# Kernel tuning notes

Hardware: AMD Instinct MI355X
Metric: run time of the kernel (lower is better)

## Reference

```python
import jax, jax.numpy as jnp
import numpy as np

N, NFEAT, NHID, NHID2 = 10000, 512, 256, 128


def setup_inputs() -> dict:
    key = jax.random.key(0)
    k1, k2, k3, k4 = jax.random.split(key, 4)
    x = jax.random.normal(k1, (N, NFEAT), dtype=jnp.float32)
    # sparse-ish row-normalized adjacency, stored dense (as the module's spmm operand)
    raw = jax.random.uniform(k2, (N, N), dtype=jnp.float32)
    adj = jnp.where(raw > 0.995, raw, 0.0)
    adj = adj / jnp.maximum(adj.sum(axis=1, keepdims=True), 1e-6)
    W1 = jax.random.normal(k3, (NFEAT, NHID), dtype=jnp.float32) / np.sqrt(NFEAT)
    b1 = jnp.zeros((NHID,), dtype=jnp.float32)
    W2 = jax.random.normal(k4, (NHID, NHID2), dtype=jnp.float32) / np.sqrt(NHID)
    b2 = jnp.zeros((NHID2,), dtype=jnp.float32)
    return {"x": x, "adj": adj, "W1": W1, "b1": b1, "W2": W2, "b2": b2}


def gcn_conv(x, adj, W, b):
    # standard Kipf GCNConv: adj @ (x @ W) + b
    return adj @ (x @ W) + b


def reference(x, adj, W1, b1, W2, b2):
    h = jax.nn.relu(gcn_conv(x, adj, W1, b1))
    # dropout is identity in inference mode (training=False)
    h = jax.nn.relu(gcn_conv(h, adj, W2, b2))
    return h
```

## Files before the change

kernel.cpp:

```cpp
#include <hip/hip_runtime.h>

#define N_NODES 10000
#define NFEAT   512
#define NHID    256
#define NHID2   128
#define CAP     128

typedef __attribute__((ext_vector_type(8))) short bf16x8;
typedef __attribute__((ext_vector_type(4))) float f32x4;
typedef __attribute__((ext_vector_type(2))) int   i32x2;

__device__ __forceinline__ ushort f2bf(float f){
  union { float f; unsigned u; } v; v.f = f;
  unsigned r = v.u + 0x7FFFu + ((v.u >> 16) & 1u);
  return (ushort)(r >> 16);
}
__device__ __forceinline__ float bf2f(ushort u){
  union { unsigned u; float f; } v; v.u = ((unsigned)u) << 16; return v.f;
}

__launch_bounds__(256)
__global__ void k_scan_cvt(const float* __restrict__ adj, const float* __restrict__ x,
                           const float* __restrict__ W1, const float* __restrict__ W2,
                           ushort* __restrict__ xb, ushort* __restrict__ w1t,
                           ushort* __restrict__ w2t, int* __restrict__ row_nnz,
                           i32x2* __restrict__ pja){
  const int b = blockIdx.x, t = threadIdx.x;

  if (b >= N_NODES){
    if (b < 15000){
      int i = ((b - N_NODES) * 256 + t) * 4;
      float4 q = *(const float4*)(x + i);
      ushort4 o; o.x = f2bf(q.x); o.y = f2bf(q.y); o.z = f2bf(q.z); o.w = f2bf(q.w);
      *(ushort4*)(xb + i) = o;
    } else if (b < 15512){
      int id = (b - 15000) * 256 + t;
      int n = id >> 9, k = id & 511;
      w1t[id] = f2bf(W1[k * NHID + n]);
    } else {
      int id = (b - 15512) * 256 + t;
      int n = id >> 8, k = id & 255;
      w2t[id] = f2bf(W2[k * NHID2 + n]);
    }
    return;
  }

  const int r = b;
  const int lane = t & 63, w = t >> 6;
  const float* row = adj + (size_t)r * N_NODES;
  __shared__ int swave[4];

  f32x4 vals[10];
  #pragma unroll
  for (int v = 0; v < 9; v++)
    vals[v] = __builtin_nontemporal_load((const f32x4*)(row + v * 1024 + t * 4));
  vals[9] = (f32x4){0.f, 0.f, 0.f, 0.f};
  if (t < 196) vals[9] = __builtin_nontemporal_load((const f32x4*)(row + 9216 + t * 4));

  int cnt = 0;
  #pragma unroll
  for (int v = 0; v < 10; v++)
    cnt += (vals[v].x != 0.f) + (vals[v].y != 0.f) + (vals[v].z != 0.f) + (vals[v].w != 0.f);

  int incl = cnt;
  #pragma unroll
  for (int d = 1; d < 64; d <<= 1){
    int u = __shfl_up(incl, d, 64);
    if (lane >= d) incl += u;
  }
  if (lane == 63) swave[w] = incl;
  __syncthreads();
  int woff = 0, total = 0;
  #pragma unroll
  for (int i = 0; i < 4; i++){
    int s = swave[i];
    total += s;
    if (i < w) woff += s;
  }
  int pos = woff + incl - cnt;

  #pragma unroll
  for (int v = 0; v < 10; v++){
    float q[4] = {vals[v].x, vals[v].y, vals[v].z, vals[v].w};
    #pragma unroll
    for (int e = 0; e < 4; e++){
      if (q[e] != 0.f && pos < CAP){
        pja[(size_t)r * CAP + pos] = (i32x2){(v * 1024 + t * 4 + e) << 8, __float_as_int(q[e])};
        pos++;
      }
    }
  }
  if (t == 0) row_nnz[r] = min(total, CAP);
}

__launch_bounds__(256)
__global__ void k_gemm1(const ushort* __restrict__ A, const ushort* __restrict__ Bt,
                        ushort* __restrict__ xw1_lo, ushort* __restrict__ xw1_hi){
  const int lane = threadIdx.x & 63;
  const int w    = threadIdx.x >> 6;
  const int wr   = w >> 1, wc = w & 1;
  const int r16  = lane & 15;
  const int kg   = lane >> 4;
  const int row0 = blockIdx.x * 64 + wr * 32;
  const int col0 = blockIdx.y * 64 + wc * 32;

  int arow[2], bcol[2];
  #pragma unroll
  for (int r = 0; r < 2; r++){
    int ar = row0 + r * 16 + r16;
    arow[r] = (ar >= N_NODES) ? (N_NODES - 1) : ar;
  }
  #pragma unroll
  for (int c = 0; c < 2; c++) bcol[c] = col0 + c * 16 + r16;

  f32x4 acc[2][2];
  #pragma unroll
  for (int r = 0; r < 2; r++)
    #pragma unroll
    for (int c = 0; c < 2; c++)
      acc[r][c] = (f32x4){0.f, 0.f, 0.f, 0.f};

  bf16x8 aA[2], bA[2], aB[2], bB[2];
  auto LOADF = [&](bf16x8* a, bf16x8* bb, int k0){
    #pragma unroll
    for (int r = 0; r < 2; r++)
      a[r] = *(const bf16x8*)(A + (size_t)arow[r] * NFEAT + k0 + kg * 8);
    #pragma unroll
    for (int c = 0; c < 2; c++)
      bb[c] = *(const bf16x8*)(Bt + (size_t)bcol[c] * NFEAT + k0 + kg * 8);
  };
  auto MM = [&](bf16x8* a, bf16x8* bb){
    #pragma unroll
    for (int r = 0; r < 2; r++)
      #pragma unroll
      for (int c = 0; c < 2; c++)
        acc[r][c] = __builtin_amdgcn_mfma_f32_16x16x32_bf16(a[r], bb[c], acc[r][c], 0, 0, 0);
  };

  LOADF(aA, bA, 0);
  #pragma unroll
  for (int k0 = 0; k0 < NFEAT; k0 += 64){
    if (k0 + 32 < NFEAT) LOADF(aB, bB, k0 + 32);
    MM(aA, bA);
    if (k0 + 64 < NFEAT) LOADF(aA, bA, k0 + 64);
    if (k0 + 32 < NFEAT) MM(aB, bB);
  }

  ushort* dst = (blockIdx.y < 2) ? xw1_lo : xw1_hi;
  const int cbase = (blockIdx.y < 2) ? 0 : 128;
  #pragma unroll
  for (int r = 0; r < 2; r++)
    #pragma unroll
    for (int c = 0; c < 2; c++){
      int col = col0 + c * 16 + r16 - cbase;
      #pragma unroll
      for (int i = 0; i < 4; i++){
        int row = row0 + r * 16 + kg * 4 + i;
        if (row < N_NODES) dst[(size_t)row * 128 + col] = f2bf(acc[r][c][i]);
      }
    }
}

__launch_bounds__(256)
__global__ void k_agg1(const int* __restrict__ row_nnz, const i32x2* __restrict__ pja,
                       const ushort* __restrict__ xw1_lo, const ushort* __restrict__ xw1_hi,
                       const float* __restrict__ b1, ushort* __restrict__ Hb){
  const int half = blockIdx.x & 1;
  const int r0   = (blockIdx.x >> 1) * 16;
  const int t = threadIdx.x;
  __shared__ i32x2 sl[16][CAP];
  __shared__ int   sn[16];
  if (t < 16) sn[t] = row_nnz[r0 + t];
  #pragma unroll
  for (int e = 0; e < 8; e++){
    int idx = t + e * 256;
    int rr = idx >> 7, kk = idx & (CAP - 1);
    sl[rr][kk] = pja[(size_t)(r0 + rr) * CAP + kk];
  }
  __syncthreads();

  const int wv = t >> 6, lane = t & 63;
  const char* table = (const char*)(half ? xw1_hi : xw1_lo);
  const float bias0 = b1[half * 128 + lane * 2 + 0];
  const float bias1 = b1[half * 128 + lane * 2 + 1];

  #pragma unroll
  for (int rr = wv; rr < 16; rr += 4){
    const int n = sn[rr];
    float a0 = 0.f, a1 = 0.f;
    for (int k = 0; k < n; k++){
      i32x2 p = sl[rr][k];
      uint pk = *(const uint*)(table + p.x + lane * 4);
      float a = __int_as_float(p.y);
      a0 += a * bf2f((ushort)(pk & 0xffff));
      a1 += a * bf2f((ushort)(pk >> 16));
    }
    uint o = ((uint)f2bf(fmaxf(a1 + bias1, 0.f)) << 16) | (uint)f2bf(fmaxf(a0 + bias0, 0.f));
    *(uint*)(Hb + (size_t)(r0 + rr) * NHID + half * 128 + lane * 2) = o;
  }
}

__launch_bounds__(256)
__global__ void k_gemm2(const ushort* __restrict__ A, const ushort* __restrict__ Bt,
                        ushort* __restrict__ C){
  const int lane = threadIdx.x & 63;
  const int w    = threadIdx.x >> 6;
  const int wr   = w >> 1, wc = w & 1;
  const int r16  = lane & 15;
  const int kg   = lane >> 4;
  const int row0 = blockIdx.x * 64 + wr * 32;
  const int col0 = blockIdx.y * 64 + wc * 32;

  int arow[2], bcol[2];
  #pragma unroll
  for (int r = 0; r < 2; r++){
    int ar = row0 + r * 16 + r16;
    arow[r] = (ar >= N_NODES) ? (N_NODES - 1) : ar;
  }
  #pragma unroll
  for (int c = 0; c < 2; c++) bcol[c] = col0 + c * 16 + r16;

  f32x4 acc[2][2];
  #pragma unroll
  for (int r = 0; r < 2; r++)
    #pragma unroll
    for (int c = 0; c < 2; c++)
      acc[r][c] = (f32x4){0.f, 0.f, 0.f, 0.f};

  bf16x8 aA[2], bA[2], aB[2], bB[2];
  auto LOADF = [&](bf16x8* a, bf16x8* bb, int k0){
    #pragma unroll
    for (int r = 0; r < 2; r++)
      a[r] = *(const bf16x8*)(A + (size_t)arow[r] * NHID + k0 + kg * 8);
    #pragma unroll
    for (int c = 0; c < 2; c++)
      bb[c] = *(const bf16x8*)(Bt + (size_t)bcol[c] * NHID + k0 + kg * 8);
  };
  auto MM = [&](bf16x8* a, bf16x8* bb){
    #pragma unroll
    for (int r = 0; r < 2; r++)
      #pragma unroll
      for (int c = 0; c < 2; c++)
        acc[r][c] = __builtin_amdgcn_mfma_f32_16x16x32_bf16(a[r], bb[c], acc[r][c], 0, 0, 0);
  };

  LOADF(aA, bA, 0);
  #pragma unroll
  for (int k0 = 0; k0 < NHID; k0 += 64){
    if (k0 + 32 < NHID) LOADF(aB, bB, k0 + 32);
    MM(aA, bA);
    if (k0 + 64 < NHID) LOADF(aA, bA, k0 + 64);
    if (k0 + 32 < NHID) MM(aB, bB);
  }

  #pragma unroll
  for (int r = 0; r < 2; r++)
    #pragma unroll
    for (int c = 0; c < 2; c++){
      int col = col0 + c * 16 + r16;
      #pragma unroll
      for (int i = 0; i < 4; i++){
        int row = row0 + r * 16 + kg * 4 + i;
        if (row < N_NODES) C[(size_t)row * NHID2 + col] = f2bf(acc[r][c][i]);
      }
    }
}

__launch_bounds__(256)
__global__ void k_agg2(const int* __restrict__ row_nnz, const i32x2* __restrict__ pja,
                       const ushort* __restrict__ hw2b, const float* __restrict__ b2,
                       float* __restrict__ out){
  const int r0 = blockIdx.x * 8;
  const int t = threadIdx.x;
  __shared__ i32x2 sl[8][CAP];
  __shared__ int   sn[8];
  if (t < 8) sn[t] = row_nnz[r0 + t];
  #pragma unroll
  for (int e = 0; e < 4; e++){
    int idx = t + e * 256;
    int rr = idx >> 7, kk = idx & (CAP - 1);
    sl[rr][kk] = pja[(size_t)(r0 + rr) * CAP + kk];
  }
  __syncthreads();

  const int wv = t >> 6, lane = t & 63;
  const char* table = (const char*)hw2b;
  const float bias0 = b2[lane * 2 + 0];
  const float bias1 = b2[lane * 2 + 1];

  #pragma unroll
  for (int rr = wv; rr < 8; rr += 4){
    const int n = sn[rr];
    float a0 = 0.f, a1 = 0.f;
    for (int k = 0; k < n; k++){
      i32x2 p = sl[rr][k];
      uint pk = *(const uint*)(table + p.x + lane * 4);
      float a = __int_as_float(p.y);
      a0 += a * bf2f((ushort)(pk & 0xffff));
      a1 += a * bf2f((ushort)(pk >> 16));
    }
    float2 o = make_float2(fmaxf(a0 + bias0, 0.f), fmaxf(a1 + bias1, 0.f));
    *(float2*)(out + (size_t)(r0 + rr) * NHID2 + lane * 2) = o;
  }
}

extern "C" void kernel_launch(void* const* d_in, const int* in_sizes, int n_in,
                              void* d_out, int out_size, void* d_ws, size_t ws_size,
                              hipStream_t stream){
  const float* x   = (const float*)d_in[0];
  const float* adj = (const float*)d_in[1];
  const float* W1  = (const float*)d_in[2];
  const float* b1  = (const float*)d_in[3];
  const float* W2  = (const float*)d_in[4];
  const float* b2  = (const float*)d_in[5];
  float* out = (float*)d_out;
  char*  ws  = (char*)d_ws;

  ushort* xb     = (ushort*)(ws);
  ushort* w1t    = (ushort*)(ws + 10240000);
  ushort* w2t    = (ushort*)(ws + 10502144);
  ushort* xw1_lo = (ushort*)(ws + 10567680);
  ushort* xw1_hi = (ushort*)(ws + 13127680);
  ushort* Hb     = (ushort*)(ws + 15687680);
  ushort* hw2b   = (ushort*)(ws + 20807680);
  int*    nnz    = (int*)(ws + 23367680);
  i32x2*  pja    = (i32x2*)(ws + 23407680);

  k_scan_cvt<<<15640, 256, 0, stream>>>(adj, x, W1, W2, xb, w1t, w2t, nnz, pja);

  k_gemm1<<<dim3(157, 4), 256, 0, stream>>>(xb, w1t, xw1_lo, xw1_hi);

  k_agg1<<<1250, 256, 0, stream>>>(nnz, pja, xw1_lo, xw1_hi, b1, Hb);

  k_gemm2<<<dim3(157, 2), 256, 0, stream>>>(Hb, w2t, hw2b);

  k_agg2<<<1250, 256, 0, stream>>>(nnz, pja, hw2b, b2, out);
}
```

Baseline: 142.0 us.

## Reassociate second GCN layer and fuse aggregation with W2 GEMM

Layer 2 is now computed as (adj @ H) @ W2 instead of adj @ (H @ W2). A single kernel gathers the sparse neighbours of 16 rows into shared memory as bf16, then multiplies that tile by W2 with MFMA and applies bias and ReLU. This removes the separate GEMM kernel launch and the write and re-read of the intermediate H·W2 buffer. In exchange, the sparse gather now runs over 256-wide rows instead of 128-wide, doubling gather bytes per nonzero, and the grid shrinks to 625 blocks.

Measured after the change: 151.4 us. +6.6%, slower.

```diff
diff --git a/kernel.cpp b/kernel.cpp
--- a/kernel.cpp
+++ b/kernel.cpp
@@ -201,82 +201,17 @@
 }
 
 __launch_bounds__(256)
-__global__ void k_gemm2(const ushort* __restrict__ A, const ushort* __restrict__ Bt,
-                        ushort* __restrict__ C){
-  const int lane = threadIdx.x & 63;
-  const int w    = threadIdx.x >> 6;
-  const int wr   = w >> 1, wc = w & 1;
-  const int r16  = lane & 15;
-  const int kg   = lane >> 4;
-  const int row0 = blockIdx.x * 64 + wr * 32;
-  const int col0 = blockIdx.y * 64 + wc * 32;
-
-  int arow[2], bcol[2];
-  #pragma unroll
-  for (int r = 0; r < 2; r++){
-    int ar = row0 + r * 16 + r16;
-    arow[r] = (ar >= N_NODES) ? (N_NODES - 1) : ar;
-  }
-  #pragma unroll
-  for (int c = 0; c < 2; c++) bcol[c] = col0 + c * 16 + r16;
-
-  f32x4 acc[2][2];
-  #pragma unroll
-  for (int r = 0; r < 2; r++)
-    #pragma unroll
-    for (int c = 0; c < 2; c++)
-      acc[r][c] = (f32x4){0.f, 0.f, 0.f, 0.f};
-
-  bf16x8 aA[2], bA[2], aB[2], bB[2];
-  auto LOADF = [&](bf16x8* a, bf16x8* bb, int k0){
-    #pragma unroll
-    for (int r = 0; r < 2; r++)
-      a[r] = *(const bf16x8*)(A + (size_t)arow[r] * NHID + k0 + kg * 8);
-    #pragma unroll
-    for (int c = 0; c < 2; c++)
-      bb[c] = *(const bf16x8*)(Bt + (size_t)bcol[c] * NHID + k0 + kg * 8);
-  };
-  auto MM = [&](bf16x8* a, bf16x8* bb){
-    #pragma unroll
-    for (int r = 0; r < 2; r++)
-      #pragma unroll
-      for (int c = 0; c < 2; c++)
-        acc[r][c] = __builtin_amdgcn_mfma_f32_16x16x32_bf16(a[r], bb[c], acc[r][c], 0, 0, 0);
-  };
-
-  LOADF(aA, bA, 0);
-  #pragma unroll
-  for (int k0 = 0; k0 < NHID; k0 += 64){
-    if (k0 + 32 < NHID) LOADF(aB, bB, k0 + 32);
-    MM(aA, bA);
-    if (k0 + 64 < NHID) LOADF(aA, bA, k0 + 64);
-    if (k0 + 32 < NHID) MM(aB, bB);
-  }
-
-  #pragma unroll
-  for (int r = 0; r < 2; r++)
-    #pragma unroll
-    for (int c = 0; c < 2; c++){
-      int col = col0 + c * 16 + r16;
-      #pragma unroll
-      for (int i = 0; i < 4; i++){
-        int row = row0 + r * 16 + kg * 4 + i;
-        if (row < N_NODES) C[(size_t)row * NHID2 + col] = f2bf(acc[r][c][i]);
-      }
-    }
-}
-
-__launch_bounds__(256)
-__global__ void k_agg2(const int* __restrict__ row_nnz, const i32x2* __restrict__ pja,
-                       const ushort* __restrict__ hw2b, const float* __restrict__ b2,
-                       float* __restrict__ out){
-  const int r0 = blockIdx.x * 8;
+__global__ void k_agg2mm(const int* __restrict__ row_nnz, const i32x2* __restrict__ pja,
+                         const ushort* __restrict__ Hb, const ushort* __restrict__ w2t,
+                         const float* __restrict__ b2, float* __restrict__ out){
+  const int r0 = blockIdx.x * 16;
   const int t = threadIdx.x;
-  __shared__ i32x2 sl[8][CAP];
-  __shared__ int   sn[8];
-  if (t < 8) sn[t] = row_nnz[r0 + t];
-  #pragma unroll
-  for (int e = 0; e < 4; e++){
+  __shared__ i32x2  sl[16][CAP];
+  __shared__ int    sn[16];
+  __shared__ ushort Gb[16][264];
+  if (t < 16) sn[t] = row_nnz[r0 + t];
+  #pragma unroll
+  for (int e = 0; e < 8; e++){
     int idx = t + e * 256;
     int rr = idx >> 7, kk = idx & (CAP - 1);
     sl[rr][kk] = pja[(size_t)(r0 + rr) * CAP + kk];
@@ -284,23 +219,46 @@
   __syncthreads();
 
   const int wv = t >> 6, lane = t & 63;
-  const char* table = (const char*)hw2b;
-  const float bias0 = b2[lane * 2 + 0];
-  const float bias1 = b2[lane * 2 + 1];
-
-  #pragma unroll
-  for (int rr = wv; rr < 8; rr += 4){
+
+  #pragma unroll
+  for (int rr = wv; rr < 16; rr += 4){
     const int n = sn[rr];
-    float a0 = 0.f, a1 = 0.f;
+    float a0 = 0.f, a1 = 0.f, a2 = 0.f, a3 = 0.f;
     for (int k = 0; k < n; k++){
       i32x2 p = sl[rr][k];
-      uint pk = *(const uint*)(table + p.x + lane * 4);
+      uint2 pk = *(const uint2*)((const char*)Hb + ((size_t)(uint)p.x << 1) + lane * 8);
       float a = __int_as_float(p.y);
-      a0 += a * bf2f((ushort)(pk & 0xffff));
-      a1 += a * bf2f((ushort)(pk >> 16));
-    }
-    float2 o = make_float2(fmaxf(a0 + bias0, 0.f), fmaxf(a1 + bias1, 0.f));
-    *(float2*)(out + (size_t)(r0 + rr) * NHID2 + lane * 2) = o;
+      a0 += a * bf2f((ushort)(pk.x & 0xffff));
+      a1 += a * bf2f((ushort)(pk.x >> 16));
+      a2 += a * bf2f((ushort)(pk.y & 0xffff));
+      a3 += a * bf2f((ushort)(pk.y >> 16));
+    }
+    uint lo = ((uint)f2bf(a1) << 16) | (uint)f2bf(a0);
+    uint hi = ((uint)f2bf(a3) << 16) | (uint)f2bf(a2);
+    *(uint2*)(&Gb[rr][lane * 4]) = make_uint2(lo, hi);
+  }
+  __syncthreads();
+
+  const int r16 = lane & 15, kg = lane >> 4;
+  int bcol[2] = { wv * 32 + r16, wv * 32 + 16 + r16 };
+  f32x4 acc[2] = { (f32x4){0.f,0.f,0.f,0.f}, (f32x4){0.f,0.f,0.f,0.f} };
+  #pragma unroll
+  for (int k0 = 0; k0 < NHID; k0 += 32){
+    bf16x8 a = *(const bf16x8*)(&Gb[r16][k0 + kg * 8]);
+    #pragma unroll
+    for (int c = 0; c < 2; c++){
+      bf16x8 bfr = *(const bf16x8*)(w2t + (size_t)bcol[c] * NHID + k0 + kg * 8);
+      acc[c] = __builtin_amdgcn_mfma_f32_16x16x32_bf16(a, bfr, acc[c], 0, 0, 0);
+    }
+  }
+  #pragma unroll
+  for (int c = 0; c < 2; c++){
+    const float bias = b2[bcol[c]];
+    #pragma unroll
+    for (int i = 0; i < 4; i++){
+      int row = r0 + kg * 4 + i;
+      out[(size_t)row * NHID2 + bcol[c]] = fmaxf(acc[c][i] + bias, 0.f);
+    }
   }
 }
 
@@ -322,9 +280,8 @@
   ushort* xw1_lo = (ushort*)(ws + 10567680);
   ushort* xw1_hi = (ushort*)(ws + 13127680);
   ushort* Hb     = (ushort*)(ws + 15687680);
-  ushort* hw2b   = (ushort*)(ws + 20807680);
-  int*    nnz    = (int*)(ws + 23367680);
-  i32x2*  pja    = (i32x2*)(ws + 23407680);
+  int*    nnz    = (int*)(ws + 20807680);
+  i32x2*  pja    = (i32x2*)(ws + 20847680);
 
   k_scan_cvt<<<15640, 256, 0, stream>>>(adj, x, W1, W2, xb, w1t, w2t, nnz, pja);
 
@@ -332,7 +289,5 @@
 
   k_agg1<<<1250, 256, 0, stream>>>(nnz, pja, xw1_lo, xw1_hi, b1, Hb);
 
-  k_gemm2<<<dim3(157, 2), 256, 0, stream>>>(Hb, w2t, hw2b);
-
-  k_agg2<<<1250, 256, 0, stream>>>(nnz, pja, hw2b, b2, out);
-}
+  k_agg2mm<<<625, 256, 0, stream>>>(nnz, pja, Hb, w2t, b2, out);
+}
```
